# Performance work log

Measured on AMD Instinct MI355X. Metric: run time of the kernel, lower is better.

The kernel has to match this reference:

```python
import jax, jax.numpy as jnp
import numpy as np
import math

B, C, H, W = 4, 256, 56, 56
RC = 32  # max(256 // 8, 8)
EPS = 1e-5


def _conv(x, w, pad):
    return jax.lax.conv_general_dilated(
        x, w, window_strides=(1, 1), padding=[(pad, pad), (pad, pad)],
        dimension_numbers=('NCHW', 'OIHW', 'NCHW'))


def setup_inputs() -> dict:
    key = jax.random.key(0)
    ks = jax.random.split(key, 9)
    s = 0.05  # keep attention logits in a sane range
    return {
        'x': jax.random.normal(ks[0], (B, C, H, W), jnp.float32),
        'wq1': jax.random.normal(ks[1], (RC, C, 1, 1), jnp.float32) * s,
        'wq3': jax.random.normal(ks[2], (RC, C, 3, 3), jnp.float32) * s,
        'wq5': jax.random.normal(ks[3], (RC, C, 5, 5), jnp.float32) * s,
        'wq7': jax.random.normal(ks[4], (RC, C, 7, 7), jnp.float32) * s,
        'wk': jax.random.normal(ks[5], (RC, C, 1, 1), jnp.float32) * s,
        'wv': jax.random.normal(ks[6], (C, C, 1, 1), jnp.float32) * s,
        'wproj': jax.random.normal(ks[7], (C, 4 * C, 1, 1), jnp.float32) * s,
        'gamma': jnp.ones((C,), jnp.float32),
        'beta': jnp.zeros((C,), jnp.float32),
    }


def reference(x, wq1, wq3, wq5, wq7, wk, wv, wproj, gamma, beta):
    b, c, h, w = x.shape
    hw = h * w
    scale = 1.0 / math.sqrt(RC)
    k = _conv(x, wk, 0).reshape(b, RC, hw)   # [B, RC, HW]
    v = _conv(x, wv, 0).reshape(b, c, hw)    # [B, C, HW]
    attended = []
    for wq, pad in ((wq1, 0), (wq3, 1), (wq5, 2), (wq7, 3)):
        q = _conv(x, wq, pad).reshape(b, RC, hw)          # [B, RC, HW]
        scores = jnp.einsum('bri,brj->bij', q, k) * scale  # [B, HW, HW]
        attn = jax.nn.softmax(scores, axis=-1)
        att = jnp.einsum('bcj,bij->bci', v, attn)          # [B, C, HW]
        attended.append(att.reshape(b, c, h, w))
    concat = jnp.concatenate(attended, axis=1)             # [B, 4C, H, W]
    out = _conv(concat, wproj, 0) + x                      # residual before BN
    # BatchNorm2d in training mode: batch stats (biased var), affine
    mean = out.mean(axis=(0, 2, 3), keepdims=True)
    var = out.var(axis=(0, 2, 3), keepdims=True)
    out = (out - mean) * jax.lax.rsqrt(var + EPS)
    return out * gamma[None, :, None, None] + beta[None, :, None, None]
```

## Files before the change

kernel.cpp:

```cpp
#include <hip/hip_runtime.h>
#include <hip/hip_bf16.h>
#include <math.h>

#define HW 3136
#define WIDTH 56
#define CC 256
#define BB 4
#define RCH 32
#define NJT (HW / 64)
#define SCLOG2E 0.2550437041556575f

using bf16x8 = __attribute__((ext_vector_type(8))) short;
using f32x4  = __attribute__((ext_vector_type(4))) float;

static __device__ __forceinline__ unsigned short f2bf(float f) {
    __hip_bfloat16 h = __float2bfloat16(f);
    return *reinterpret_cast<unsigned short*>(&h);
}

__global__ __launch_bounds__(256) void prep_weights(
    const float* __restrict__ wq3, const float* __restrict__ wq5,
    const float* __restrict__ wq7, const float* __restrict__ wproj,
    const float* __restrict__ wk, const float* __restrict__ wq1,
    const float* __restrict__ wv,
    unsigned short* __restrict__ Wb3, unsigned short* __restrict__ Wb5,
    unsigned short* __restrict__ Wb7, unsigned short* __restrict__ Wpb,
    unsigned short* __restrict__ Wkq, unsigned short* __restrict__ Wvb) {
    int e = blockIdx.x * 256 + threadIdx.x;
    if (e < 73728) {
        int c = e & 255, r = (e >> 8) & 31, t = e >> 13;
        Wb3[e] = f2bf(wq3[((size_t)r * 256 + c) * 9 + t]);
    } else if (e < 278528) {
        int i = e - 73728;
        int c = i & 255, r = (i >> 8) & 31, t = i >> 13;
        Wb5[i] = f2bf(wq5[((size_t)r * 256 + c) * 25 + t]);
    } else if (e < 679936) {
        int i = e - 278528;
        int c = i & 255, r = (i >> 8) & 31, t = i >> 13;
        Wb7[i] = f2bf(wq7[((size_t)r * 256 + c) * 49 + t]);
    } else if (e < 942080) {
        int i = e - 679936;
        Wpb[i] = f2bf(wproj[i]);
    } else if (e < 958464) {
        int i = e - 942080;
        Wkq[i] = f2bf(i < 8192 ? wk[i] : wq1[i - 8192]);
    } else if (e < 1024000) {
        int i = e - 958464;
        Wvb[i] = f2bf(wv[i]);
    }
}

__global__ __launch_bounds__(256) void transpose_x(
    const float* __restrict__ x, unsigned short* __restrict__ xT) {
    __shared__ unsigned short tile[32][33];
    const int b = blockIdx.z;
    const int i0 = blockIdx.x * 32, c0 = blockIdx.y * 32;
    const int tx = threadIdx.x & 31, ty = threadIdx.x >> 5;
    #pragma unroll
    for (int k = 0; k < 4; ++k)
        tile[ty + k * 8][tx] = f2bf(x[((size_t)b * CC + c0 + ty + k * 8) * HW + i0 + tx]);
    __syncthreads();
    #pragma unroll
    for (int k = 0; k < 4; ++k)
        xT[((size_t)b * HW + i0 + ty + k * 8) * 256 + c0 + tx] = tile[tx][ty + k * 8];
}

__global__ __launch_bounds__(256) void qk32_mfma(
    const unsigned short* __restrict__ xT, const unsigned short* __restrict__ Wkq,
    unsigned short* __restrict__ Kt, unsigned short* __restrict__ Qt) {
    const int b = blockIdx.y, z = blockIdx.z;
    const int i0 = blockIdx.x * 64;
    const int t = threadIdx.x;
    const int lane = t & 63, w = t >> 6, lg = lane >> 4, li = lane & 15;

    unsigned short* outp = z == 0 ? Kt : Qt;
    const float osc = z == 0 ? 1.0f : SCLOG2E;
    const unsigned short* wb = Wkq + z * 8192;
    const unsigned short* xb = xT + ((size_t)b * HW + i0 + w * 16 + li) * 256;

    const f32x4 z4 = (f32x4){0.f, 0.f, 0.f, 0.f};
    f32x4 acc[2] = {z4, z4};

    for (int c0 = 0; c0 < 256; c0 += 32) {
        bf16x8 ax = *(const bf16x8*)(xb + c0 + lg * 8);
        #pragma unroll
        for (int rs = 0; rs < 2; ++rs) {
            bf16x8 bw = *(const bf16x8*)(wb + (size_t)(rs * 16 + li) * 256 + c0 + lg * 8);
            acc[rs] = __builtin_amdgcn_mfma_f32_16x16x32_bf16(ax, bw, acc[rs], 0, 0, 0);
        }
    }
    unsigned short* qb = outp + ((size_t)b * HW + i0 + w * 16 + lg * 4) * 32;
    #pragma unroll
    for (int rs = 0; rs < 2; ++rs)
        #pragma unroll
        for (int r = 0; r < 4; ++r)
            qb[(size_t)r * 32 + rs * 16 + li] = f2bf(acc[rs][r] * osc);
}

__global__ __launch_bounds__(256) void v_mfma(
    const unsigned short* __restrict__ xT, const unsigned short* __restrict__ Wvb,
    unsigned short* __restrict__ Vb) {
    const int b = blockIdx.y;
    const int i0 = blockIdx.x * 32;
    const int t = threadIdx.x;
    const int lane = t & 63, w = t >> 6, lg = lane >> 4, li = lane & 15;

    const f32x4 z4 = (f32x4){0.f, 0.f, 0.f, 0.f};
    f32x4 acc[4][2];
    #pragma unroll
    for (int ct = 0; ct < 4; ++ct) { acc[ct][0] = z4; acc[ct][1] = z4; }

    const unsigned short* xb = xT + (size_t)b * HW * 256;

    for (int c0 = 0; c0 < 256; c0 += 32) {
        bf16x8 bx[2];
        #pragma unroll
        for (int is = 0; is < 2; ++is)
            bx[is] = *(const bf16x8*)(xb + (size_t)(i0 + is * 16 + li) * 256 + c0 + lg * 8);
        #pragma unroll
        for (int ct = 0; ct < 4; ++ct) {
            bf16x8 aw = *(const bf16x8*)(
                Wvb + (size_t)(w * 64 + ct * 16 + li) * 256 + c0 + lg * 8);
            #pragma unroll
            for (int is = 0; is < 2; ++is)
                acc[ct][is] = __builtin_amdgcn_mfma_f32_16x16x32_bf16(
                    aw, bx[is], acc[ct][is], 0, 0, 0);
        }
    }
    #pragma unroll
    for (int ct = 0; ct < 4; ++ct)
        #pragma unroll
        for (int is = 0; is < 2; ++is)
            #pragma unroll
            for (int r = 0; r < 4; ++r)
                Vb[((size_t)b * CC + w * 64 + ct * 16 + lg * 4 + r) * HW +
                   i0 + is * 16 + li] = f2bf(acc[ct][is][r]);
}

template <int KS>
static __device__ __forceinline__ void qconv_body(
    const unsigned short* __restrict__ xT,
    const unsigned short* __restrict__ Wb,
    unsigned short* __restrict__ q,
    unsigned short (*xs)[40]) {
    constexpr int P = (KS - 1) / 2;
    constexpr int KT = KS * KS;
    constexpr int ROWS = 64 + 114 * P;
    const int b = blockIdx.y;
    const int i0 = blockIdx.x * 64;
    const int t = threadIdx.x;
    const int lane = t & 63;
    const int w = t >> 6;
    const int li = lane & 15;
    const int lg = lane >> 4;

    const int base = i0 - P * 57;
    const int mycol = (i0 + w * 16 + li) % WIDTH;

    f32x4 acc[2];
    acc[0] = (f32x4){0.f, 0.f, 0.f, 0.f};
    acc[1] = (f32x4){0.f, 0.f, 0.f, 0.f};

    const unsigned short* xTb = xT + (size_t)b * HW * 256;

    for (int c0 = 0; c0 < 256; c0 += 32) {
        __syncthreads();
        for (int e = t; e < ROWS * 4; e += 256) {
            int row = e >> 2, cs = e & 3;
            int gidx = base + row;
            uint4 val = make_uint4(0, 0, 0, 0);
            if (gidx >= 0 && gidx < HW)
                val = *(const uint4*)(xTb + (size_t)gidx * 256 + c0 + cs * 8);
            *(uint4*)(&xs[row][cs * 8]) = val;
        }
        __syncthreads();

        #pragma unroll
        for (int tap = 0; tap < KT; ++tap) {
            const int dx = tap % KS - P;
            const int poff = (tap / KS) * WIDTH + tap % KS;
            bf16x8 a = *(const bf16x8*)(&xs[w * 16 + li + poff][lg * 8]);
            if ((unsigned)(mycol + dx) >= (unsigned)WIDTH)
                a = (bf16x8){0, 0, 0, 0, 0, 0, 0, 0};
            const unsigned short* wrow =
                Wb + (size_t)tap * 32 * 256 + c0 + lg * 8;
            bf16x8 b0 = *(const bf16x8*)(wrow + (size_t)li * 256);
            bf16x8 b1 = *(const bf16x8*)(wrow + (size_t)(16 + li) * 256);
            acc[0] = __builtin_amdgcn_mfma_f32_16x16x32_bf16(a, b0, acc[0], 0, 0, 0);
            acc[1] = __builtin_amdgcn_mfma_f32_16x16x32_bf16(a, b1, acc[1], 0, 0, 0);
        }
    }

    unsigned short* qb = q + ((size_t)b * HW + i0 + w * 16 + lg * 4) * 32;
    #pragma unroll
    for (int rs = 0; rs < 2; ++rs)
        #pragma unroll
        for (int r = 0; r < 4; ++r)
            qb[(size_t)r * 32 + rs * 16 + li] = f2bf(acc[rs][r] * SCLOG2E);
}

__global__ __launch_bounds__(256) void qconv_all(
    const unsigned short* __restrict__ xT,
    const unsigned short* __restrict__ Wb3,
    const unsigned short* __restrict__ Wb5,
    const unsigned short* __restrict__ Wb7,
    unsigned short* __restrict__ Qt) {
    __shared__ unsigned short xs[406][40];
    const size_t QSLICE = (size_t)BB * HW * 32;
    if (blockIdx.z == 0)      qconv_body<3>(xT, Wb3, Qt + 1 * QSLICE, xs);
    else if (blockIdx.z == 1) qconv_body<5>(xT, Wb5, Qt + 2 * QSLICE, xs);
    else                      qconv_body<7>(xT, Wb7, Qt + 3 * QSLICE, xs);
}

__global__ __launch_bounds__(256) void flashmfma(
    const unsigned short* __restrict__ Qt, const unsigned short* __restrict__ Kt,
    const unsigned short* __restrict__ Vb, unsigned short* __restrict__ ATTt) {
    const int F = blockIdx.x;
    const int xcd = F & 7;
    const int within = F >> 3;
    const int pair = xcd + 8 * (within / 49);
    const int b = pair & 3;
    const int g = pair >> 2;
    const int i0 = (within % 49) * 64;

    const int t = threadIdx.x;
    const int lane = t & 63;
    const int w = t >> 6;
    const int lg = lane >> 4;
    const int li = lane & 15;

    __shared__ __align__(16) unsigned short Ps[64][72];
    __shared__ float lls[64];

    const bf16x8 aq = *(const bf16x8*)(
        Qt + ((size_t)(g * BB + b) * HW + i0 + w * 16 + li) * 32 + lg * 8);

    const f32x4 z4 = (f32x4){0.f, 0.f, 0.f, 0.f};
    f32x4 acc[4][4];
    #pragma unroll
    for (int ct = 0; ct < 4; ++ct)
        #pragma unroll
        for (int is = 0; is < 4; ++is) acc[ct][is] = z4;

    float lsum[4] = {0.f, 0.f, 0.f, 0.f};

    const unsigned short* Kb = Kt + (size_t)b * HW * 32;
    const unsigned short* Vw = Vb + ((size_t)b * CC + w * 64) * HW;

    for (int jt = 0; jt < NJT; ++jt) {
        const int j0 = jt * 64;

        bf16x8 vf[4][2];
        #pragma unroll
        for (int ct = 0; ct < 4; ++ct) {
            vf[ct][0] = *(const bf16x8*)(
                Vw + (size_t)(ct * 16 + li) * HW + j0 + lg * 8);
            vf[ct][1] = *(const bf16x8*)(
                Vw + (size_t)(ct * 16 + li) * HW + j0 + 32 + lg * 8);
        }

        f32x4 S[4];
        #pragma unroll
        for (int j2 = 0; j2 < 4; ++j2) {
            bf16x8 bk = *(const bf16x8*)(Kb + (size_t)(j0 + j2 * 16 + li) * 32 + lg * 8);
            S[j2] = __builtin_amdgcn_mfma_f32_16x16x32_bf16(aq, bk, z4, 0, 0, 0);
        }

        unsigned int pk0[4], pk1[4];
        #pragma unroll
        for (int r = 0; r < 4; ++r) {
            float p0 = __builtin_amdgcn_exp2f(S[0][r]);
            float p1 = __builtin_amdgcn_exp2f(S[1][r]);
            float p2 = __builtin_amdgcn_exp2f(S[2][r]);
            float p3 = __builtin_amdgcn_exp2f(S[3][r]);
            lsum[r] += (p0 + p1) + (p2 + p3);
            asm("v_cvt_pk_bf16_f32 %0, %1, %2" : "=v"(pk0[r]) : "v"(p0), "v"(p1));
            asm("v_cvt_pk_bf16_f32 %0, %1, %2" : "=v"(pk1[r]) : "v"(p2), "v"(p3));
        }

        __syncthreads();
        #pragma unroll
        for (int r = 0; r < 4; ++r) {
            const int row = w * 16 + lg * 4 + r;
            Ps[row][li]      = (unsigned short)pk0[r];
            Ps[row][16 + li] = (unsigned short)(pk0[r] >> 16);
            Ps[row][32 + li] = (unsigned short)pk1[r];
            Ps[row][48 + li] = (unsigned short)(pk1[r] >> 16);
        }
        __syncthreads();

        bf16x8 bp[4][2];
        #pragma unroll
        for (int is = 0; is < 4; ++is)
            #pragma unroll
            for (int ks = 0; ks < 2; ++ks)
                bp[is][ks] = *(const bf16x8*)(&Ps[is * 16 + li][ks * 32 + lg * 8]);

        __builtin_amdgcn_s_setprio(1);
        #pragma unroll
        for (int ct = 0; ct < 4; ++ct) {
            #pragma unroll
            for (int is = 0; is < 4; ++is) {
                acc[ct][is] = __builtin_amdgcn_mfma_f32_16x16x32_bf16(
                    vf[ct][0], bp[is][0], acc[ct][is], 0, 0, 0);
                acc[ct][is] = __builtin_amdgcn_mfma_f32_16x16x32_bf16(
                    vf[ct][1], bp[is][1], acc[ct][is], 0, 0, 0);
            }
        }
        __builtin_amdgcn_s_setprio(0);
    }

    #pragma unroll
    for (int r = 0; r < 4; ++r) {
        float s = lsum[r];
        #pragma unroll
        for (int off = 1; off < 16; off <<= 1) s += __shfl_xor(s, off);
        if (li == 0) lls[w * 16 + lg * 4 + r] = s;
    }
    __syncthreads();

    float invl[4];
    #pragma unroll
    for (int is = 0; is < 4; ++is) invl[is] = 1.f / lls[is * 16 + li];

    #pragma unroll
    for (int ct = 0; ct < 4; ++ct)
        #pragma unroll
        for (int is = 0; is < 4; ++is) {
            float v0 = acc[ct][is][0] * invl[is];
            float v1 = acc[ct][is][1] * invl[is];
            float v2 = acc[ct][is][2] * invl[is];
            float v3 = acc[ct][is][3] * invl[is];
            unsigned int lo, hi;
            asm("v_cvt_pk_bf16_f32 %0, %1, %2" : "=v"(lo) : "v"(v0), "v"(v1));
            asm("v_cvt_pk_bf16_f32 %0, %1, %2" : "=v"(hi) : "v"(v2), "v"(v3));
            uint2 pk; pk.x = lo; pk.y = hi;
            *(uint2*)(ATTt + ((size_t)b * HW + i0 + is * 16 + li) * 1024 +
                      g * 256 + w * 64 + ct * 16 + lg * 4) = pk;
        }
}

__global__ __launch_bounds__(256) void gemm_proj(
    const unsigned short* __restrict__ ATTt, const unsigned short* __restrict__ Wpb,
    const float* __restrict__ x, float* __restrict__ out) {
    const int b = blockIdx.y;
    const int i0 = blockIdx.x * 32;
    const int t = threadIdx.x;
    const int lane = t & 63;
    const int w = t >> 6;
    const int lg = lane >> 4;
    const int li = lane & 15;

    const f32x4 z4 = (f32x4){0.f, 0.f, 0.f, 0.f};
    f32x4 acc[4][2];
    #pragma unroll
    for (int ct = 0; ct < 4; ++ct) { acc[ct][0] = z4; acc[ct][1] = z4; }

    const unsigned short* ab = ATTt + (size_t)b * HW * 1024;

    for (int k0 = 0; k0 < 1024; k0 += 32) {
        bf16x8 afr[2];
        #pragma unroll
        for (int is = 0; is < 2; ++is)
            afr[is] = *(const bf16x8*)(
                ab + (size_t)(i0 + is * 16 + li) * 1024 + k0 + lg * 8);
        #pragma unroll
        for (int ct = 0; ct < 4; ++ct) {
            bf16x8 wf = *(const bf16x8*)(
                Wpb + (size_t)(w * 64 + ct * 16 + li) * 1024 + k0 + lg * 8);
            #pragma unroll
            for (int is = 0; is < 2; ++is)
                acc[ct][is] = __builtin_amdgcn_mfma_f32_16x16x32_bf16(
                    wf, afr[is], acc[ct][is], 0, 0, 0);
        }
    }

    #pragma unroll
    for (int ct = 0; ct < 4; ++ct)
        #pragma unroll
        for (int is = 0; is < 2; ++is)
            #pragma unroll
            for (int r = 0; r < 4; ++r) {
                int co = w * 64 + ct * 16 + lg * 4 + r;
                size_t o = ((size_t)b * CC + co) * HW + i0 + is * 16 + li;
                out[o] = acc[ct][is][r] + x[o];
            }
}

__global__ __launch_bounds__(256) void bnstats(
    const float* __restrict__ out, float* __restrict__ mean,
    float* __restrict__ rstd) {
    const int c = blockIdx.x;
    float s = 0.f, s2 = 0.f;
    for (int e = threadIdx.x; e < BB * HW; e += 256) {
        int b = e / HW, i = e - b * HW;
        float v = out[((size_t)b * CC + c) * HW + i];
        s += v; s2 += v * v;
    }
    __shared__ float rs[256], rs2[256];
    rs[threadIdx.x] = s; rs2[threadIdx.x] = s2;
    __syncthreads();
    for (int st = 128; st > 0; st >>= 1) {
        if (threadIdx.x < st) {
            rs[threadIdx.x] += rs[threadIdx.x + st];
            rs2[threadIdx.x] += rs2[threadIdx.x + st];
        }
        __syncthreads();
    }
    if (threadIdx.x == 0) {
        const float n = (float)(BB * HW);
        float m = rs[0] / n;
        float var = rs2[0] / n - m * m;
        mean[c] = m;
        rstd[c] = rsqrtf(var + 1e-5f);
    }
}

__global__ __launch_bounds__(256) void bnapply(
    float* __restrict__ out, const float* __restrict__ mean,
    const float* __restrict__ rstd, const float* __restrict__ gamma,
    const float* __restrict__ beta) {
    size_t idx = (size_t)blockIdx.x * 256 + threadIdx.x;
    if (idx < (size_t)BB * CC * HW) {
        int c = (int)((idx / HW) % CC);
        out[idx] = (out[idx] - mean[c]) * rstd[c] * gamma[c] + beta[c];
    }
}

extern "C" void kernel_launch(void* const* d_in, const int* in_sizes, int n_in,
                              void* d_out, int out_size, void* d_ws, size_t ws_size,
                              hipStream_t stream) {
    const float* x     = (const float*)d_in[0];
    const float* wq1   = (const float*)d_in[1];
    const float* wq3   = (const float*)d_in[2];
    const float* wq5   = (const float*)d_in[3];
    const float* wq7   = (const float*)d_in[4];
    const float* wk    = (const float*)d_in[5];
    const float* wv    = (const float*)d_in[6];
    const float* wproj = (const float*)d_in[7];
    const float* gamma = (const float*)d_in[8];
    const float* beta  = (const float*)d_in[9];
    float* out = (float*)d_out;

    unsigned short* ATTt = (unsigned short*)d_ws;
    unsigned short* Kt   = ATTt + (size_t)BB * 4 * CC * HW;
    unsigned short* Qt   = Kt + (size_t)BB * HW * 32;
    unsigned short* Vb   = Qt + (size_t)4 * BB * HW * 32;
    unsigned short* xT   = Vb + (size_t)BB * CC * HW;
    unsigned short* Wb3  = xT + (size_t)BB * HW * CC;
    unsigned short* Wb5  = Wb3 + (size_t)9 * 32 * 256;
    unsigned short* Wb7  = Wb5 + (size_t)25 * 32 * 256;
    unsigned short* Wpb  = Wb7 + (size_t)49 * 32 * 256;
    unsigned short* Wkq  = Wpb + (size_t)256 * 1024;
    unsigned short* Wvb  = Wkq + (size_t)2 * 32 * 256;
    float* mean = (float*)(Wvb + (size_t)256 * 256);
    float* rstd = mean + CC;

    dim3 blk(256);

    prep_weights<<<dim3(4000), blk, 0, stream>>>(
        wq3, wq5, wq7, wproj, wk, wq1, wv, Wb3, Wb5, Wb7, Wpb, Wkq, Wvb);
    transpose_x<<<dim3(HW / 32, CC / 32, BB), blk, 0, stream>>>(x, xT);

    qk32_mfma<<<dim3(HW / 64, BB, 2), blk, 0, stream>>>(xT, Wkq, Kt, Qt);
    v_mfma<<<dim3(HW / 32, BB), blk, 0, stream>>>(xT, Wvb, Vb);

    qconv_all<<<dim3(HW / 64, BB, 3), blk, 0, stream>>>(xT, Wb3, Wb5, Wb7, Qt);

    flashmfma<<<dim3(8 * 2 * (HW / 64)), blk, 0, stream>>>(Qt, Kt, Vb, ATTt);

    gemm_proj<<<dim3(HW / 32, BB), blk, 0, stream>>>(ATTt, Wpb, x, out);

    bnstats<<<dim3(CC), blk, 0, stream>>>(out, mean, rstd);
    bnapply<<<dim3((BB * CC * HW + 255) / 256), blk, 0, stream>>>(out, mean, rstd, gamma, beta);
}
```

Before: 496.1 us.

## Split flash attention over key range and combine partial sums in new kernel

Splits the key loop of the attention kernel into two halves (25 and 24 tiles), doubling the grid to 1568 blocks. Each half writes unnormalized bf16 partial outputs and per-row exp sums, and a new combine kernel adds the two halves and divides by the total sum. This relies on the softmax having no running max (fixed exponent base), so the partials can simply be summed. The aim is better CU occupancy and load balance. The cost is an extra bf16 round trip of the large attention buffer, an additional kernel launch, and extra bf16 rounding of the partials.

Measured after the change: 486.0 us. 2.0% less time.

```diff
diff --git a/kernel.cpp b/kernel.cpp
--- a/kernel.cpp
+++ b/kernel.cpp
@@ -8,6 +8,7 @@
 #define BB 4
 #define RCH 32
 #define NJT (HW / 64)
+#define TSPLIT 25
 #define SCLOG2E 0.2550437041556575f
 
 using bf16x8 = __attribute__((ext_vector_type(8))) short;
@@ -214,14 +215,17 @@
 
 __global__ __launch_bounds__(256) void flashmfma(
     const unsigned short* __restrict__ Qt, const unsigned short* __restrict__ Kt,
-    const unsigned short* __restrict__ Vb, unsigned short* __restrict__ ATTt) {
+    const unsigned short* __restrict__ Vb, unsigned short* __restrict__ P0,
+    unsigned short* __restrict__ P1, float* __restrict__ Lsum) {
     const int F = blockIdx.x;
     const int xcd = F & 7;
     const int within = F >> 3;
-    const int pair = xcd + 8 * (within / 49);
+    const int q4 = within / 49;
+    const int i0 = (within % 49) * 64;
+    const int pair = xcd + 8 * (q4 & 1);
+    const int split = q4 >> 1;
     const int b = pair & 3;
     const int g = pair >> 2;
-    const int i0 = (within % 49) * 64;
 
     const int t = threadIdx.x;
     const int lane = t & 63;
@@ -230,7 +234,6 @@
     const int li = lane & 15;
 
     __shared__ __align__(16) unsigned short Ps[64][72];
-    __shared__ float lls[64];
 
     const bf16x8 aq = *(const bf16x8*)(
         Qt + ((size_t)(g * BB + b) * HW + i0 + w * 16 + li) * 32 + lg * 8);
@@ -247,7 +250,10 @@
     const unsigned short* Kb = Kt + (size_t)b * HW * 32;
     const unsigned short* Vw = Vb + ((size_t)b * CC + w * 64) * HW;
 
-    for (int jt = 0; jt < NJT; ++jt) {
+    const int jt0 = split == 0 ? 0 : TSPLIT;
+    const int jt1 = split == 0 ? TSPLIT : NJT;
+
+    for (int jt = jt0; jt < jt1; ++jt) {
         const int j0 = jt * 64;
 
         bf16x8 vf[4][2];
@@ -315,29 +321,57 @@
         float s = lsum[r];
         #pragma unroll
         for (int off = 1; off < 16; off <<= 1) s += __shfl_xor(s, off);
-        if (li == 0) lls[w * 16 + lg * 4 + r] = s;
-    }
-    __syncthreads();
-
-    float invl[4];
-    #pragma unroll
-    for (int is = 0; is < 4; ++is) invl[is] = 1.f / lls[is * 16 + li];
-
+        if (li == 0)
+            Lsum[(size_t)split * 16 * HW + (size_t)(g * BB + b) * HW +
+                 i0 + w * 16 + lg * 4 + r] = s;
+    }
+
+    unsigned short* Pp = split == 0 ? P0 : P1;
     #pragma unroll
     for (int ct = 0; ct < 4; ++ct)
         #pragma unroll
         for (int is = 0; is < 4; ++is) {
-            float v0 = acc[ct][is][0] * invl[is];
-            float v1 = acc[ct][is][1] * invl[is];
-            float v2 = acc[ct][is][2] * invl[is];
-            float v3 = acc[ct][is][3] * invl[is];
             unsigned int lo, hi;
-            asm("v_cvt_pk_bf16_f32 %0, %1, %2" : "=v"(lo) : "v"(v0), "v"(v1));
-            asm("v_cvt_pk_bf16_f32 %0, %1, %2" : "=v"(hi) : "v"(v2), "v"(v3));
+            asm("v_cvt_pk_bf16_f32 %0, %1, %2"
+                : "=v"(lo) : "v"(acc[ct][is][0]), "v"(acc[ct][is][1]));
+            asm("v_cvt_pk_bf16_f32 %0, %1, %2"
+                : "=v"(hi) : "v"(acc[ct][is][2]), "v"(acc[ct][is][3]));
             uint2 pk; pk.x = lo; pk.y = hi;
-            *(uint2*)(ATTt + ((size_t)b * HW + i0 + is * 16 + li) * 1024 +
+            *(uint2*)(Pp + ((size_t)b * HW + i0 + is * 16 + li) * 1024 +
                       g * 256 + w * 64 + ct * 16 + lg * 4) = pk;
         }
+}
+
+__global__ __launch_bounds__(256) void combine_att(
+    unsigned short* __restrict__ Pio, const unsigned short* __restrict__ P1,
+    const float* __restrict__ Lsum) {
+    const int b = blockIdx.y;
+    const int hw = blockIdx.x * 2 + (threadIdx.x >> 7);
+    const int lp = threadIdx.x & 127;
+    const int c0 = lp * 8;
+    const int g = c0 >> 8;
+
+    const size_t lidx = (size_t)(g * BB + b) * HW + hw;
+    const float invl = 1.f / (Lsum[lidx] + Lsum[(size_t)16 * HW + lidx]);
+
+    const size_t off = ((size_t)b * HW + hw) * 1024 + c0;
+    uint4 ua = *(const uint4*)(Pio + off);
+    uint4 ub = *(const uint4*)(P1 + off);
+    unsigned int a[4] = {ua.x, ua.y, ua.z, ua.w};
+    unsigned int bb[4] = {ub.x, ub.y, ub.z, ub.w};
+    unsigned int o[4];
+    #pragma unroll
+    for (int k = 0; k < 4; ++k) {
+        float a0 = __uint_as_float(a[k] << 16);
+        float a1 = __uint_as_float(a[k] & 0xffff0000u);
+        float b0 = __uint_as_float(bb[k] << 16);
+        float b1 = __uint_as_float(bb[k] & 0xffff0000u);
+        float f0 = (a0 + b0) * invl;
+        float f1 = (a1 + b1) * invl;
+        asm("v_cvt_pk_bf16_f32 %0, %1, %2" : "=v"(o[k]) : "v"(f0), "v"(f1));
+    }
+    uint4 uo; uo.x = o[0]; uo.y = o[1]; uo.z = o[2]; uo.w = o[3];
+    *(uint4*)(Pio + off) = uo;
 }
 
 __global__ __launch_bounds__(256) void gemm_proj(
@@ -442,8 +476,10 @@
     const float* beta  = (const float*)d_in[9];
     float* out = (float*)d_out;
 
-    unsigned short* ATTt = (unsigned short*)d_ws;
-    unsigned short* Kt   = ATTt + (size_t)BB * 4 * CC * HW;
+    unsigned short* P0   = (unsigned short*)d_ws;
+    unsigned short* P1   = P0 + (size_t)BB * HW * 1024;
+    float* Lsum          = (float*)(P1 + (size_t)BB * HW * 1024);
+    unsigned short* Kt   = (unsigned short*)(Lsum + (size_t)2 * 16 * HW);
     unsigned short* Qt   = Kt + (size_t)BB * HW * 32;
     unsigned short* Vb   = Qt + (size_t)4 * BB * HW * 32;
     unsigned short* xT   = Vb + (size_t)BB * CC * HW;
@@ -467,9 +503,10 @@
 
     qconv_all<<<dim3(HW / 64, BB, 3), blk, 0, stream>>>(xT, Wb3, Wb5, Wb7, Qt);
 
-    flashmfma<<<dim3(8 * 2 * (HW / 64)), blk, 0, stream>>>(Qt, Kt, Vb, ATTt);
-
-    gemm_proj<<<dim3(HW / 32, BB), blk, 0, stream>>>(ATTt, Wpb, x, out);
+    flashmfma<<<dim3(8 * 4 * (HW / 64)), blk, 0, stream>>>(Qt, Kt, Vb, P0, P1, Lsum);
+    combine_att<<<dim3(HW / 2, BB), blk, 0, stream>>>(P0, P1, Lsum);
+
+    gemm_proj<<<dim3(HW / 32, BB), blk, 0, stream>>>(P0, Wpb, x, out);
 
     bnstats<<<dim3(CC), blk, 0, stream>>>(out, mean, rstd);
     bnapply<<<dim3((BB * CC * HW + 255) / 256), blk, 0, stream>>>(out, mean, rstd, gamma, beta);
```
